# Performance work log

Hardware: AMD Instinct MI355X
Metric: run time of the kernel (lower is better)

## Reference

```python
import jax, jax.numpy as jnp
import numpy as np

BITWIDTH = 8  # args.actBitwidth


def setup_inputs() -> dict:
    key = jax.random.key(0)
    k1, k2, k3 = jax.random.split(key, 3)
    x = jax.random.normal(k1, (32, 256, 56, 56), dtype=jnp.float32)
    # orthonormal-ish projection matrix (stand-in for PCA eigenvectors)
    u = jax.random.normal(k2, (256, 256), dtype=jnp.float32) / np.float32(np.sqrt(256.0))
    # positive per-channel clamp values
    clamp_val = jax.random.uniform(k3, (256,), dtype=jnp.float32) * 3.0 + 0.5
    return {"x": x, "u": u, "clamp_val": clamp_val}


def reference(x, u, clamp_val):
    N, C, H, W = x.shape
    x = jax.nn.relu(x)
    # [C, N*H*W] channel-major flatten (matches transpose(0,1).view(C,-1))
    im = jnp.transpose(x, (1, 0, 2, 3)).reshape(C, -1)
    mn = jnp.mean(im, axis=1, keepdims=True)
    im = im - mn
    # PCA projection
    p = u.T @ im  # [C, NHW]
    # per-channel symmetric clamp
    c = clamp_val[:, None]
    pq = jnp.clip(p, -c, c)
    # per-channel dynamic min/max uniform quantization (fused over channels)
    dmax = jnp.max(pq, axis=1, keepdims=True)
    dmin = jnp.min(pq, axis=1, keepdims=True)
    rng = dmax - dmin
    scale = (2.0 ** BITWIDTH - 1.0) / jnp.where(rng == 0, 1.0, rng)
    q = jnp.round((pq - dmin) * scale) / scale + dmin
    q = jnp.where(rng == 0, pq, q)
    # project back, re-center, add channel means
    out = u @ q
    out = out - jnp.mean(out, axis=1, keepdims=True) + mn
    return jnp.transpose(out.reshape(C, N, H, W), (1, 0, 2, 3))
```

## Files before the change

### kernel.cpp

```cpp
#include <hip/hip_runtime.h>
#include <hip/hip_bf16.h>
#include <stdint.h>

#define CH    256
#define HWsz  3136
#define NIMG  32
#define COLS  (NIMG * HWsz)
#define KB    32
#define TN    64
#define TILES (COLS / TN)
#define NBINS 8
#define CHUNK (TN * 20)

typedef float  f32x4  __attribute__((ext_vector_type(4)));
typedef __bf16 bf16x8 __attribute__((ext_vector_type(8)));

struct Stats {
  float mnsum[NBINS][CH];
  float mn[CH];
  float poff[CH];
  float clF[CH];
  unsigned dminK[NBINS][CH];
  unsigned dmaxK[NBINS][CH];
  float dminF[CH];
  float scaleF[CH];
  float invF[CH];
  float qsum[CH];
  float corr[CH];
  unsigned short u_bf[CH * CH];
  unsigned short uT_bf[CH * CH];
};

__device__ __forceinline__ unsigned short f2bf(float f) {
  union { float f; unsigned u; } v; v.f = f;
  unsigned r = v.u + 0x7fffu + ((v.u >> 16) & 1u);
  return (unsigned short)(r >> 16);
}
__device__ __forceinline__ float bf2f(unsigned short b) {
  union { unsigned u; float f; } v; v.u = ((unsigned)b) << 16;
  return v.f;
}
__device__ __forceinline__ unsigned pack_bf2(float a, float b) {
  return (unsigned)f2bf(a) | ((unsigned)f2bf(b) << 16);
}
__device__ __forceinline__ unsigned fkey(float f) {
  unsigned u = __float_as_uint(f);
  return (u & 0x80000000u) ? ~u : (u | 0x80000000u);
}
__device__ __forceinline__ float funkey(unsigned k) {
  unsigned u = (k & 0x80000000u) ? (k & 0x7fffffffu) : ~k;
  return __uint_as_float(u);
}
__device__ __forceinline__ float clampf(float v, float c) {
  return fminf(fmaxf(v, -c), c);
}
__device__ __forceinline__ float dq(float v, float dmin, float sc, float inv) {
  return sc == 0.f ? v : fmaf(rintf((v - dmin) * sc), inv, dmin);
}

__global__ void k_init(const float* __restrict__ u, Stats* st) {
  int b = blockIdx.x, t = threadIdx.x;
  st->u_bf[b * CH + t]  = f2bf(u[b * CH + t]);
  st->uT_bf[b * CH + t] = f2bf(u[t * CH + b]);
  if (b < NBINS) {
    st->mnsum[b][t] = 0.f;
    st->dminK[b][t] = 0xFFFFFFFFu;
    st->dmaxK[b][t] = 0u;
  }
  if (b == 0) st->qsum[t] = 0.f;
}

__global__ __launch_bounds__(256, 4) void k_gemm1(const float* __restrict__ x,
                                                  Stats* __restrict__ st,
                                                  unsigned* __restrict__ pq,
                                                  long nstride) {
  __shared__ __align__(16) unsigned ldsU[8 * CHUNK];

  const int t = threadIdx.x;
  const int lane = t & 63, wv = t >> 6;
  const int g = t & 15, cpair = t >> 4;
  const int c2 = cpair & 3;
  const int q = lane >> 4, r15 = lane & 15;
  const int wsw = (((wv ^ ((g >> 1) & 3)) << 2) | c2);

  const int tile = blockIdx.x;
  const int n = tile / 49, hw0 = (tile % 49) * TN;
  const unsigned short* uT = st->uT_bf;
  const int bin = blockIdx.x & (NBINS - 1);

  float4 rA[4], rB[4];
  float relp[8][2] = {};

  const float* pbase = x + (size_t)n * CH * HWsz + (size_t)(2 * cpair) * HWsz + hw0 + 4 * g;

  auto ld4 = [&](int h) {
#pragma unroll
    for (int i = 0; i < 4; ++i) {
      const float* p = pbase + (size_t)((4 * h + i) * KB) * HWsz;
      rA[i] = *(const float4*)p;
      rB[i] = *(const float4*)(p + HWsz);
    }
  };
  auto stage4 = [&](int h) {
#pragma unroll
    for (int i = 0; i < 4; ++i) {
      const int kc = 4 * h + i;
      const float a[4] = {fmaxf(rA[i].x, 0.f), fmaxf(rA[i].y, 0.f),
                          fmaxf(rA[i].z, 0.f), fmaxf(rA[i].w, 0.f)};
      const float b[4] = {fmaxf(rB[i].x, 0.f), fmaxf(rB[i].y, 0.f),
                          fmaxf(rB[i].z, 0.f), fmaxf(rB[i].w, 0.f)};
      relp[kc][0] += (a[0] + a[1]) + (a[2] + a[3]);
      relp[kc][1] += (b[0] + b[1]) + (b[2] + b[3]);
      unsigned* dst = ldsU + kc * CHUNK;
#pragma unroll
      for (int j = 0; j < 4; ++j)
        dst[(4 * g + j) * 20 + wsw] = pack_bf2(a[j], b[j]);
    }
  };

  ld4(0);
  stage4(0);
  ld4(1);
  stage4(1);
  __syncthreads();

  f32x4 acc[4][4];
#pragma unroll
  for (int mt = 0; mt < 4; ++mt)
#pragma unroll
    for (int nt = 0; nt < 4; ++nt)
      acc[mt][nt] = (f32x4)(0.f);

#pragma unroll
  for (int kc = 0; kc < 8; ++kc) {
    bf16x8 afr[4];
#pragma unroll
    for (int mt = 0; mt < 4; ++mt)
      afr[mt] = *(const bf16x8*)(uT + (64 * wv + 16 * mt + r15) * CH + kc * KB + q * 8);
    bf16x8 bfr[4];
#pragma unroll
    for (int nt = 0; nt < 4; ++nt) {
      const int j = nt * 16 + r15;
      bfr[nt] = *(const bf16x8*)((const unsigned short*)(ldsU + kc * CHUNK) +
                                 (size_t)j * 40 + ((q ^ ((j >> 3) & 3)) << 3));
    }
#pragma unroll
    for (int nt = 0; nt < 4; ++nt)
#pragma unroll
      for (int mt = 0; mt < 4; ++mt)
        acc[mt][nt] = __builtin_amdgcn_mfma_f32_16x16x32_bf16(afr[mt], bfr[nt], acc[mt][nt], 0, 0, 0);
  }

#pragma unroll
  for (int mt = 0; mt < 4; ++mt) {
    const int kp0 = 32 * wv + 8 * mt + 2 * q;
    float mn4[4], mx4[4];
#pragma unroll
    for (int nt = 0; nt < 4; ++nt) {
      const unsigned w01 = pack_bf2(acc[mt][nt][0], acc[mt][nt][1]);
      const unsigned w23 = pack_bf2(acc[mt][nt][2], acc[mt][nt][3]);
      const size_t base = (size_t)n * nstride + (size_t)kp0 * HWsz + hw0 + nt * 16 + r15;
      pq[base]        = w01;
      pq[base + HWsz] = w23;
      const float v[4] = {bf2f((unsigned short)(w01 & 0xffffu)), bf2f((unsigned short)(w01 >> 16)),
                          bf2f((unsigned short)(w23 & 0xffffu)), bf2f((unsigned short)(w23 >> 16))};
#pragma unroll
      for (int reg = 0; reg < 4; ++reg) {
        if (nt == 0) { mn4[reg] = v[reg]; mx4[reg] = v[reg]; }
        else { mn4[reg] = fminf(mn4[reg], v[reg]); mx4[reg] = fmaxf(mx4[reg], v[reg]); }
      }
    }
#pragma unroll
    for (int reg = 0; reg < 4; ++reg) {
#pragma unroll
      for (int m = 8; m; m >>= 1) {
        mn4[reg] = fminf(mn4[reg], __shfl_xor(mn4[reg], m));
        mx4[reg] = fmaxf(mx4[reg], __shfl_xor(mx4[reg], m));
      }
      if (r15 == 0) {
        const int row = 64 * wv + 16 * mt + 4 * q + reg;
        atomicMin(&st->dminK[bin][row], fkey(mn4[reg]));
        atomicMax(&st->dmaxK[bin][row], fkey(mx4[reg]));
      }
    }
  }

  __syncthreads();
  float (*scr)[17] = (float (*)[17])ldsU;
#pragma unroll
  for (int kc = 0; kc < 8; ++kc) {
    scr[kc * 32 + 2 * cpair + 0][g] = relp[kc][0];
    scr[kc * 32 + 2 * cpair + 1][g] = relp[kc][1];
  }
  __syncthreads();
  float s = 0.f;
#pragma unroll
  for (int i = 0; i < 16; ++i) s += scr[t][i];
  atomicAdd(&st->mnsum[bin][t], s);
}

__global__ void k_finalize(const float* __restrict__ u,
                           const float* __restrict__ clampv, Stats* st) {
  int t = threadIdx.x;
  __shared__ float smn[CH];
  float msum = 0.f;
  unsigned kmin = 0xFFFFFFFFu, kmax = 0u;
#pragma unroll
  for (int b = 0; b < NBINS; ++b) {
    msum += st->mnsum[b][t];
    unsigned a = st->dminK[b][t], z = st->dmaxK[b][t];
    kmin = (a < kmin) ? a : kmin;
    kmax = (z > kmax) ? z : kmax;
  }
  float mnv = msum * (1.f / COLS);
  st->mn[t] = mnv;
  smn[t] = mnv;
  __syncthreads();
  float acc = 0.f;
  for (int c = 0; c < CH; ++c) acc += u[c * CH + t] * smn[c];
  st->poff[t] = acc;
  float cv = clampv[t];
  st->clF[t] = cv;
  float dmin = clampf(funkey(kmin) - acc, cv);
  float dmax = clampf(funkey(kmax) - acc, cv);
  float rng = dmax - dmin;
  float sc = 0.f, iv = 0.f;
  if (rng != 0.f) { sc = 255.f / rng; iv = rng / 255.f; }
  st->dminF[t] = dmin; st->scaleF[t] = sc; st->invF[t] = iv;
}

__global__ __launch_bounds__(256) void k_qsum(const unsigned* __restrict__ pq,
                                              long nstride,
                                              Stats* __restrict__ st) {
  __shared__ float w4a[4], w4b[4];
  const int blk = blockIdx.x;
  const int n = blk >> 7, kp = blk & 127;
  const int r0 = 2 * kp, r1 = r0 + 1;
  const float p0 = st->poff[r0], c0 = st->clF[r0], d0 = st->dminF[r0],
              sc0 = st->scaleF[r0], i0 = st->invF[r0];
  const float p1 = st->poff[r1], c1 = st->clF[r1], d1 = st->dminF[r1],
              sc1 = st->scaleF[r1], i1 = st->invF[r1];
  const uint4* p = (const uint4*)(pq + (size_t)n * nstride + (size_t)kp * HWsz);
  float s0 = 0.f, s1 = 0.f;
  for (int i = threadIdx.x; i < HWsz / 4; i += 256) {
    const uint4 w = p[i];
    const unsigned ws[4] = {w.x, w.y, w.z, w.w};
#pragma unroll
    for (int k = 0; k < 4; ++k) {
      s0 += dq(clampf(bf2f((unsigned short)(ws[k] & 0xffffu)) - p0, c0), d0, sc0, i0);
      s1 += dq(clampf(bf2f((unsigned short)(ws[k] >> 16)) - p1, c1), d1, sc1, i1);
    }
  }
  for (int off = 32; off; off >>= 1) {
    s0 += __shfl_down(s0, off);
    s1 += __shfl_down(s1, off);
  }
  int lane = threadIdx.x & 63, wvi = threadIdx.x >> 6;
  if (!lane) { w4a[wvi] = s0; w4b[wvi] = s1; }
  __syncthreads();
  if (threadIdx.x == 0) {
    atomicAdd(&st->qsum[r0], (w4a[0] + w4a[1]) + (w4a[2] + w4a[3]));
    atomicAdd(&st->qsum[r1], (w4b[0] + w4b[1]) + (w4b[2] + w4b[3]));
  }
}

__global__ void k_corr(const float* __restrict__ u, Stats* st) {
  int t = threadIdx.x;
  __shared__ float qm[CH];
  qm[t] = st->qsum[t] * (1.f / COLS);
  __syncthreads();
  float acc = 0.f;
  for (int r = 0; r < CH; ++r) acc += u[t * CH + r] * qm[r];
  st->corr[t] = st->mn[t] - acc;
}

__global__ __launch_bounds__(256, 4) void k_gemm2(const unsigned* __restrict__ pq,
                                                  long nstride,
                                                  Stats* __restrict__ st,
                                                  float* __restrict__ out) {
  __shared__ __align__(16) unsigned ldsU[8 * CHUNK];
  __shared__ float pf[CH], cl[CH], dm[CH], sc[CH], iv[CH];

  const int t = threadIdx.x;
  const int lane = t & 63, wv = t >> 6;
  const int g = t & 15, kpl = t >> 4;
  const int c2 = kpl & 3;
  const int q = lane >> 4, r15 = lane & 15;
  const int wsw = (((wv ^ ((g >> 1) & 3)) << 2) | c2);

  const int tile = blockIdx.x;
  const int n = tile / 49, hw0 = (tile % 49) * TN;
  const unsigned short* uA = st->u_bf;

  pf[t] = st->poff[t]; cl[t] = st->clF[t]; dm[t] = st->dminF[t];
  sc[t] = st->scaleF[t]; iv[t] = st->invF[t];
  __syncthreads();

  uint4 rW[8];
  const unsigned* p0g = pq + (size_t)n * nstride + (size_t)kpl * HWsz + hw0 + 4 * g;
#pragma unroll
  for (int kc = 0; kc < 8; ++kc)
    rW[kc] = *(const uint4*)(p0g + (size_t)(kc * 16) * HWsz);

#pragma unroll
  for (int kc = 0; kc < 8; ++kc) {
    const int R0 = 2 * (kc * 16 + kpl);
    const float pp0 = pf[R0],     q0 = cl[R0],     e0 = dm[R0],     s0 = sc[R0],     v0 = iv[R0];
    const float pp1 = pf[R0 + 1], q1 = cl[R0 + 1], e1 = dm[R0 + 1], s1 = sc[R0 + 1], v1 = iv[R0 + 1];
    const unsigned ws[4] = {rW[kc].x, rW[kc].y, rW[kc].z, rW[kc].w};
    unsigned* dst = ldsU + kc * CHUNK;
#pragma unroll
    for (int i = 0; i < 4; ++i) {
      const float a = dq(clampf(bf2f((unsigned short)(ws[i] & 0xffffu)) - pp0, q0), e0, s0, v0);
      const float b = dq(clampf(bf2f((unsigned short)(ws[i] >> 16)) - pp1, q1), e1, s1, v1);
      dst[(4 * g + i) * 20 + wsw] = pack_bf2(a, b);
    }
  }
  __syncthreads();

  f32x4 acc[4][4];
#pragma unroll
  for (int mt = 0; mt < 4; ++mt)
#pragma unroll
    for (int nt = 0; nt < 4; ++nt)
      acc[mt][nt] = (f32x4)(0.f);

#pragma unroll
  for (int kc = 0; kc < 8; ++kc) {
    bf16x8 afr[4];
#pragma unroll
    for (int mt = 0; mt < 4; ++mt)
      afr[mt] = *(const bf16x8*)(uA + (64 * wv + 16 * mt + r15) * CH + kc * KB + q * 8);
    bf16x8 bfr[4];
#pragma unroll
    for (int nt = 0; nt < 4; ++nt) {
      const int j = nt * 16 + r15;
      bfr[nt] = *(const bf16x8*)((const unsigned short*)(ldsU + kc * CHUNK) +
                                 (size_t)j * 40 + ((q ^ ((j >> 3) & 3)) << 3));
    }
#pragma unroll
    for (int nt = 0; nt < 4; ++nt)
#pragma unroll
      for (int mt = 0; mt < 4; ++mt)
        acc[mt][nt] = __builtin_amdgcn_mfma_f32_16x16x32_bf16(afr[mt], bfr[nt], acc[mt][nt], 0, 0, 0);
  }

#pragma unroll
  for (int mt = 0; mt < 4; ++mt)
#pragma unroll
    for (int reg = 0; reg < 4; ++reg) {
      const int row = 64 * wv + 16 * mt + 4 * q + reg;
      const float cr = st->corr[row];
      const size_t obase = ((size_t)n * CH + row) * HWsz + hw0;
#pragma unroll
      for (int nt = 0; nt < 4; ++nt)
        out[obase + nt * 16 + r15] = acc[mt][nt][reg] + cr;
    }
}

extern "C" void kernel_launch(void* const* d_in, const int* in_sizes, int n_in,
                              void* d_out, int out_size, void* d_ws, size_t ws_size,
                              hipStream_t stream) {
  const float* x  = (const float*)d_in[0];
  const float* u  = (const float*)d_in[1];
  const float* cv = (const float*)d_in[2];
  float* out = (float*)d_out;
  Stats* st = (Stats*)d_ws;

  const size_t pq_off = (sizeof(Stats) + 255) & ~(size_t)255;
  const size_t pq_bytes = (size_t)NIMG * (CH / 2) * HWsz * 4;
  unsigned* pq;
  long nstride;
  if (ws_size >= pq_off + pq_bytes) {
    pq = (unsigned*)((char*)d_ws + pq_off);
    nstride = (long)(CH / 2) * HWsz;
  } else {
    pq = (unsigned*)d_out + (size_t)(CH / 2) * HWsz;
    nstride = (long)CH * HWsz;
  }

  k_init<<<CH, CH, 0, stream>>>(u, st);
  k_gemm1<<<TILES, 256, 0, stream>>>(x, st, pq, nstride);
  k_finalize<<<1, CH, 0, stream>>>(u, cv, st);
  k_qsum<<<NIMG * (CH / 2), 256, 0, stream>>>(pq, nstride, st);
  k_corr<<<1, CH, 0, stream>>>(u, st);
  k_gemm2<<<TILES, 256, 0, stream>>>(pq, nstride, st, out);
}
```

Measured before the change: 322.7 us.

## Use 512-thread blocks in both GEMM kernels, splitting rows across 8 waves

Both GEMM kernels now launch 512 threads per tile instead of 256. Each thread loads and stages half the K-chunks, and each of the 8 waves computes 32 output rows instead of 64. This halves per-thread accumulator and load-register pressure and adds more waves per tile to hide global-load latency. The cost is more waves sharing the same LDS tile and extra barrier overhead. The launch_bounds minimum-occupancy hint is also removed.

New measurement: 285.9 us. 1.13x faster.

```diff
diff --git a/kernel.cpp b/kernel.cpp
--- a/kernel.cpp
+++ b/kernel.cpp
@@ -70,18 +70,18 @@
   if (b == 0) st->qsum[t] = 0.f;
 }
 
-__global__ __launch_bounds__(256, 4) void k_gemm1(const float* __restrict__ x,
-                                                  Stats* __restrict__ st,
-                                                  unsigned* __restrict__ pq,
-                                                  long nstride) {
+__global__ __launch_bounds__(512)
+void k_gemm1(const float* __restrict__ x,
+             Stats* __restrict__ st,
+             unsigned* __restrict__ pq,
+             long nstride) {
   __shared__ __align__(16) unsigned ldsU[8 * CHUNK];
 
   const int t = threadIdx.x;
   const int lane = t & 63, wv = t >> 6;
-  const int g = t & 15, cpair = t >> 4;
-  const int c2 = cpair & 3;
+  const int g = t & 15, cp = (t >> 4) & 15, half = t >> 8;
   const int q = lane >> 4, r15 = lane & 15;
-  const int wsw = (((wv ^ ((g >> 1) & 3)) << 2) | c2);
+  const int wsw = (((cp >> 2) ^ ((g >> 1) & 3)) << 2) | (cp & 3);
 
   const int tile = blockIdx.x;
   const int n = tile / 49, hw0 = (tile % 49) * TN;
@@ -89,54 +89,44 @@
   const int bin = blockIdx.x & (NBINS - 1);
 
   float4 rA[4], rB[4];
-  float relp[8][2] = {};
-
-  const float* pbase = x + (size_t)n * CH * HWsz + (size_t)(2 * cpair) * HWsz + hw0 + 4 * g;
-
-  auto ld4 = [&](int h) {
-#pragma unroll
-    for (int i = 0; i < 4; ++i) {
-      const float* p = pbase + (size_t)((4 * h + i) * KB) * HWsz;
-      rA[i] = *(const float4*)p;
-      rB[i] = *(const float4*)(p + HWsz);
-    }
-  };
-  auto stage4 = [&](int h) {
-#pragma unroll
-    for (int i = 0; i < 4; ++i) {
-      const int kc = 4 * h + i;
-      const float a[4] = {fmaxf(rA[i].x, 0.f), fmaxf(rA[i].y, 0.f),
-                          fmaxf(rA[i].z, 0.f), fmaxf(rA[i].w, 0.f)};
-      const float b[4] = {fmaxf(rB[i].x, 0.f), fmaxf(rB[i].y, 0.f),
-                          fmaxf(rB[i].z, 0.f), fmaxf(rB[i].w, 0.f)};
-      relp[kc][0] += (a[0] + a[1]) + (a[2] + a[3]);
-      relp[kc][1] += (b[0] + b[1]) + (b[2] + b[3]);
-      unsigned* dst = ldsU + kc * CHUNK;
-#pragma unroll
-      for (int j = 0; j < 4; ++j)
-        dst[(4 * g + j) * 20 + wsw] = pack_bf2(a[j], b[j]);
-    }
-  };
-
-  ld4(0);
-  stage4(0);
-  ld4(1);
-  stage4(1);
-  __syncthreads();
-
-  f32x4 acc[4][4];
-#pragma unroll
-  for (int mt = 0; mt < 4; ++mt)
+  float relp[4][2] = {};
+
+  const float* pbase = x + (size_t)n * CH * HWsz + (size_t)(2 * cp) * HWsz + hw0 + 4 * g;
+#pragma unroll
+  for (int i = 0; i < 4; ++i) {
+    const float* p = pbase + (size_t)((4 * half + i) * KB) * HWsz;
+    rA[i] = *(const float4*)p;
+    rB[i] = *(const float4*)(p + HWsz);
+  }
+#pragma unroll
+  for (int i = 0; i < 4; ++i) {
+    const int kc = 4 * half + i;
+    const float a[4] = {fmaxf(rA[i].x, 0.f), fmaxf(rA[i].y, 0.f),
+                        fmaxf(rA[i].z, 0.f), fmaxf(rA[i].w, 0.f)};
+    const float b[4] = {fmaxf(rB[i].x, 0.f), fmaxf(rB[i].y, 0.f),
+                        fmaxf(rB[i].z, 0.f), fmaxf(rB[i].w, 0.f)};
+    relp[i][0] += (a[0] + a[1]) + (a[2] + a[3]);
+    relp[i][1] += (b[0] + b[1]) + (b[2] + b[3]);
+    unsigned* dst = ldsU + kc * CHUNK;
+#pragma unroll
+    for (int j = 0; j < 4; ++j)
+      dst[(4 * g + j) * 20 + wsw] = pack_bf2(a[j], b[j]);
+  }
+  __syncthreads();
+
+  f32x4 acc[2][4];
+#pragma unroll
+  for (int mt = 0; mt < 2; ++mt)
 #pragma unroll
     for (int nt = 0; nt < 4; ++nt)
       acc[mt][nt] = (f32x4)(0.f);
 
 #pragma unroll
   for (int kc = 0; kc < 8; ++kc) {
-    bf16x8 afr[4];
-#pragma unroll
-    for (int mt = 0; mt < 4; ++mt)
-      afr[mt] = *(const bf16x8*)(uT + (64 * wv + 16 * mt + r15) * CH + kc * KB + q * 8);
+    bf16x8 afr[2];
+#pragma unroll
+    for (int mt = 0; mt < 2; ++mt)
+      afr[mt] = *(const bf16x8*)(uT + (32 * wv + 16 * mt + r15) * CH + kc * KB + q * 8);
     bf16x8 bfr[4];
 #pragma unroll
     for (int nt = 0; nt < 4; ++nt) {
@@ -147,13 +137,13 @@
 #pragma unroll
     for (int nt = 0; nt < 4; ++nt)
 #pragma unroll
-      for (int mt = 0; mt < 4; ++mt)
+      for (int mt = 0; mt < 2; ++mt)
         acc[mt][nt] = __builtin_amdgcn_mfma_f32_16x16x32_bf16(afr[mt], bfr[nt], acc[mt][nt], 0, 0, 0);
   }
 
 #pragma unroll
-  for (int mt = 0; mt < 4; ++mt) {
-    const int kp0 = 32 * wv + 8 * mt + 2 * q;
+  for (int mt = 0; mt < 2; ++mt) {
+    const int kp0 = 16 * wv + 8 * mt + 2 * q;
     float mn4[4], mx4[4];
 #pragma unroll
     for (int nt = 0; nt < 4; ++nt) {
@@ -178,7 +168,7 @@
         mx4[reg] = fmaxf(mx4[reg], __shfl_xor(mx4[reg], m));
       }
       if (r15 == 0) {
-        const int row = 64 * wv + 16 * mt + 4 * q + reg;
+        const int row = 32 * wv + 16 * mt + 4 * q + reg;
         atomicMin(&st->dminK[bin][row], fkey(mn4[reg]));
         atomicMax(&st->dmaxK[bin][row], fkey(mx4[reg]));
       }
@@ -188,15 +178,18 @@
   __syncthreads();
   float (*scr)[17] = (float (*)[17])ldsU;
 #pragma unroll
-  for (int kc = 0; kc < 8; ++kc) {
-    scr[kc * 32 + 2 * cpair + 0][g] = relp[kc][0];
-    scr[kc * 32 + 2 * cpair + 1][g] = relp[kc][1];
-  }
-  __syncthreads();
-  float s = 0.f;
-#pragma unroll
-  for (int i = 0; i < 16; ++i) s += scr[t][i];
-  atomicAdd(&st->mnsum[bin][t], s);
+  for (int i = 0; i < 4; ++i) {
+    const int kc = 4 * half + i;
+    scr[kc * KB + 2 * cp + 0][g] = relp[i][0];
+    scr[kc * KB + 2 * cp + 1][g] = relp[i][1];
+  }
+  __syncthreads();
+  if (t < CH) {
+    float s = 0.f;
+#pragma unroll
+    for (int i = 0; i < 16; ++i) s += scr[t][i];
+    atomicAdd(&st->mnsum[bin][t], s);
+  }
 }
 
 __global__ void k_finalize(const float* __restrict__ u,
@@ -274,63 +267,66 @@
   st->corr[t] = st->mn[t] - acc;
 }
 
-__global__ __launch_bounds__(256, 4) void k_gemm2(const unsigned* __restrict__ pq,
-                                                  long nstride,
-                                                  Stats* __restrict__ st,
-                                                  float* __restrict__ out) {
+__global__ __launch_bounds__(512)
+void k_gemm2(const unsigned* __restrict__ pq,
+             long nstride,
+             Stats* __restrict__ st,
+             float* __restrict__ out) {
   __shared__ __align__(16) unsigned ldsU[8 * CHUNK];
   __shared__ float pf[CH], cl[CH], dm[CH], sc[CH], iv[CH];
 
   const int t = threadIdx.x;
   const int lane = t & 63, wv = t >> 6;
-  const int g = t & 15, kpl = t >> 4;
-  const int c2 = kpl & 3;
+  const int g = t & 15, kpl = (t >> 4) & 15, half = t >> 8;
   const int q = lane >> 4, r15 = lane & 15;
-  const int wsw = (((wv ^ ((g >> 1) & 3)) << 2) | c2);
+  const int wsw = (((kpl >> 2) ^ ((g >> 1) & 3)) << 2) | (kpl & 3);
 
   const int tile = blockIdx.x;
   const int n = tile / 49, hw0 = (tile % 49) * TN;
   const unsigned short* uA = st->u_bf;
 
-  pf[t] = st->poff[t]; cl[t] = st->clF[t]; dm[t] = st->dminF[t];
-  sc[t] = st->scaleF[t]; iv[t] = st->invF[t];
-  __syncthreads();
-
-  uint4 rW[8];
+  if (t < CH) {
+    pf[t] = st->poff[t]; cl[t] = st->clF[t]; dm[t] = st->dminF[t];
+    sc[t] = st->scaleF[t]; iv[t] = st->invF[t];
+  }
+  __syncthreads();
+
+  uint4 rW[4];
   const unsigned* p0g = pq + (size_t)n * nstride + (size_t)kpl * HWsz + hw0 + 4 * g;
 #pragma unroll
-  for (int kc = 0; kc < 8; ++kc)
-    rW[kc] = *(const uint4*)(p0g + (size_t)(kc * 16) * HWsz);
-
-#pragma unroll
-  for (int kc = 0; kc < 8; ++kc) {
+  for (int i = 0; i < 4; ++i)
+    rW[i] = *(const uint4*)(p0g + (size_t)((4 * half + i) * 16) * HWsz);
+
+#pragma unroll
+  for (int i = 0; i < 4; ++i) {
+    const int kc = 4 * half + i;
     const int R0 = 2 * (kc * 16 + kpl);
     const float pp0 = pf[R0],     q0 = cl[R0],     e0 = dm[R0],     s0 = sc[R0],     v0 = iv[R0];
     const float pp1 = pf[R0 + 1], q1 = cl[R0 + 1], e1 = dm[R0 + 1], s1 = sc[R0 + 1], v1 = iv[R0 + 1];
-    const unsigned ws[4] = {rW[kc].x, rW[kc].y, rW[kc].z, rW[kc].w};
+    const unsigned ws[4] = {rW[i].x, rW[i].y, rW[i].z, rW[i].w};
     unsigned* dst = ldsU + kc * CHUNK;
 #pragma unroll
-    for (int i = 0; i < 4; ++i) {
-      const float a = dq(clampf(bf2f((unsigned short)(ws[i] & 0xffffu)) - pp0, q0), e0, s0, v0);
-      const float b = dq(clampf(bf2f((unsigned short)(ws[i] >> 16)) - pp1, q1), e1, s1, v1);
-      dst[(4 * g + i) * 20 + wsw] = pack_bf2(a, b);
-    }
-  }
-  __syncthreads();
-
-  f32x4 acc[4][4];
-#pragma unroll
-  for (int mt = 0; mt < 4; ++mt)
+    for (int j = 0; j < 4; ++j) {
+      const float a = dq(clampf(bf2f((unsigned short)(ws[j] & 0xffffu)) - pp0, q0), e0, s0, v0);
+      const float b = dq(clampf(bf2f((unsigned short)(ws[j] >> 16)) - pp1, q1), e1, s1, v1);
+      dst[(4 * g + j) * 20 + wsw] = pack_bf2(a, b);
+    }
+  }
+  __syncthreads();
+
+  f32x4 acc[2][4];
+#pragma unroll
+  for (int mt = 0; mt < 2; ++mt)
 #pragma unroll
     for (int nt = 0; nt < 4; ++nt)
       acc[mt][nt] = (f32x4)(0.f);
 
 #pragma unroll
   for (int kc = 0; kc < 8; ++kc) {
-    bf16x8 afr[4];
-#pragma unroll
-    for (int mt = 0; mt < 4; ++mt)
-      afr[mt] = *(const bf16x8*)(uA + (64 * wv + 16 * mt + r15) * CH + kc * KB + q * 8);
+    bf16x8 afr[2];
+#pragma unroll
+    for (int mt = 0; mt < 2; ++mt)
+      afr[mt] = *(const bf16x8*)(uA + (32 * wv + 16 * mt + r15) * CH + kc * KB + q * 8);
     bf16x8 bfr[4];
 #pragma unroll
     for (int nt = 0; nt < 4; ++nt) {
@@ -341,15 +337,15 @@
 #pragma unroll
     for (int nt = 0; nt < 4; ++nt)
 #pragma unroll
-      for (int mt = 0; mt < 4; ++mt)
+      for (int mt = 0; mt < 2; ++mt)
         acc[mt][nt] = __builtin_amdgcn_mfma_f32_16x16x32_bf16(afr[mt], bfr[nt], acc[mt][nt], 0, 0, 0);
   }
 
 #pragma unroll
-  for (int mt = 0; mt < 4; ++mt)
+  for (int mt = 0; mt < 2; ++mt)
 #pragma unroll
     for (int reg = 0; reg < 4; ++reg) {
-      const int row = 64 * wv + 16 * mt + 4 * q + reg;
+      const int row = 32 * wv + 16 * mt + 4 * q + reg;
       const float cr = st->corr[row];
       const size_t obase = ((size_t)n * CH + row) * HWsz + hw0;
 #pragma unroll
@@ -380,9 +376,9 @@
   }
 
   k_init<<<CH, CH, 0, stream>>>(u, st);
-  k_gemm1<<<TILES, 256, 0, stream>>>(x, st, pq, nstride);
+  k_gemm1<<<TILES, 512, 0, stream>>>(x, st, pq, nstride);
   k_finalize<<<1, CH, 0, stream>>>(u, cv, st);
   k_qsum<<<NIMG * (CH / 2), 256, 0, stream>>>(pq, nstride, st);
   k_corr<<<1, CH, 0, stream>>>(u, st);
-  k_gemm2<<<TILES, 256, 0, stream>>>(pq, nstride, st, out);
-}
+  k_gemm2<<<TILES, 512, 0, stream>>>(pq, nstride, st, out);
+}
```
